# Optimization experiments

Measured on AMD Instinct MI355X. Metric: run time of the kernel, lower is better.

Reference implementation:

```python
import jax, jax.numpy as jnp
import numpy as np
import math

ANCHORS = np.array([[12., 16.], [19., 36.], [40., 28.]], dtype=np.float32)
NUM_CLASSES = 80
IMG_DIM = 608.0
NUM_ANCHORS = 3


def setup_inputs() -> dict:
    key = jax.random.key(0)
    ks = jax.random.split(key, 9)
    B, A, G, NC = 16, NUM_ANCHORS, 76, NUM_CLASSES
    x = jax.random.normal(ks[0], (B, A * (NC + 5), G, G), jnp.float32)
    iou = jax.random.uniform(ks[1], (B, A, G, G), jnp.float32, 0.0, 0.95)
    obj_mask = jax.random.bernoulli(ks[2], 0.02, (B, A, G, G))
    noobj_mask = jnp.logical_and(~obj_mask, jax.random.bernoulli(ks[3], 0.95, (B, A, G, G)))
    tw = jax.random.uniform(ks[4], (B, A, G, G), jnp.float32, 0.1, 4.0)
    th = jax.random.uniform(ks[5], (B, A, G, G), jnp.float32, 0.1, 4.0)
    tcls = jax.random.uniform(ks[6], (B, A, G, G, NC), jnp.float32)
    tconf = jax.random.uniform(ks[7], (B, A, G, G), jnp.float32)
    tb = jax.random.uniform(ks[8], (B, A, G, G, 4), jnp.float32)
    # target boxes in grid units: centers in [0,G), sizes in (0.5, 8.5)
    target_boxes = jnp.concatenate([tb[..., :2] * G, tb[..., 2:] * 8.0 + 0.5], -1)
    return {"x": x, "iou": iou, "obj_mask": obj_mask, "noobj_mask": noobj_mask,
            "tw": tw, "th": th, "tcls": tcls, "tconf": tconf, "target_boxes": target_boxes}


def _clog(p):
    # torch F.binary_cross_entropy clamps log to -100
    return jnp.maximum(jnp.log(p), -100.0)


def _bce(p, t):
    return -(t * _clog(p) + (1.0 - t) * _clog(1.0 - p))


def yolo_forward(x, iou, obj_mask, noobj_mask, tw, th, tcls, tconf, target_boxes):
    B = x.shape[0]
    G = x.shape[2]
    A, NC = NUM_ANCHORS, NUM_CLASSES
    stride = IMG_DIM / G
    # [B, A, G, G, 5+NC]
    pred = x.reshape(B, A, NC + 5, G, G).transpose(0, 1, 3, 4, 2)
    px = jax.nn.sigmoid(pred[..., 0])
    py = jax.nn.sigmoid(pred[..., 1])
    pw = pred[..., 2]
    ph = pred[..., 3]
    pconf = jax.nn.sigmoid(pred[..., 4])
    pcls = jax.nn.sigmoid(pred[..., 5:])

    scaled = jnp.asarray(ANCHORS) / stride
    gx = jnp.arange(G, dtype=x.dtype)[None, None, None, :]
    gy = jnp.arange(G, dtype=x.dtype)[None, None, :, None]
    aw = scaled[:, 0][None, :, None, None]
    ah = scaled[:, 1][None, :, None, None]

    bx = px + gx
    by = py + gy
    bw = jnp.exp(pw) * aw
    bh = jnp.exp(ph) * ah
    pred_boxes = jnp.stack([bx, by, bw, bh], -1)

    output = jnp.concatenate([
        pred_boxes.reshape(B, -1, 4) * stride,
        pconf.reshape(B, -1, 1),
        pcls.reshape(B, -1, NC)], -1)

    # ---- loss (masked CIoU + BCE), computed dense then mask-reduced ----
    m = obj_mask.astype(x.dtype)
    nm = noobj_mask.astype(x.dtype)
    txc, tyc, twd, tht = (target_boxes[..., i] for i in range(4))

    tx1, ty1 = txc - twd / 2, tyc - tht / 2
    tx2, ty2 = txc + twd / 2, tyc + tht / 2
    px1, py1 = bx - bw / 2, by - bh / 2
    px2, py2 = bx + bw / 2, by + bh / 2

    xc1 = jnp.minimum(px1, tx1)
    yc1 = jnp.minimum(py1, ty1)
    xc2 = jnp.maximum(px2, tx2)
    yc2 = jnp.maximum(py2, ty2)

    c = (xc2 - xc1) ** 2 + (yc2 - yc1) ** 2 + 1e-07
    d = (txc - bx) ** 2 + (tyc - by) ** 2
    rDIoU = d / c
    v = (4.0 / math.pi ** 2) * (jnp.arctan(tw / th) - jnp.arctan(pw / ph)) ** 2
    S = 1.0 - iou
    alpha = jax.lax.stop_gradient(v / (S + v))  # torch.no_grad() block
    ciou_term = 1.0 - iou + rDIoU + alpha * v
    CIoUloss = jnp.sum(m * ciou_term) / B

    cnt_obj = jnp.maximum(jnp.sum(m), 1.0)
    cnt_noobj = jnp.maximum(jnp.sum(nm), 1.0)
    bce_conf = _bce(pconf, tconf)
    loss_conf = 1.0 * jnp.sum(m * bce_conf) / cnt_obj + 100.0 * jnp.sum(nm * bce_conf) / cnt_noobj
    loss_cls = jnp.sum(m[..., None] * _bce(pcls, tcls)) / (cnt_obj * NUM_CLASSES)

    total_loss = CIoUloss + loss_conf + loss_cls
    return output, total_loss


def reference(x, iou, obj_mask, noobj_mask, tw, th, tcls, tconf, target_boxes):
    return yolo_forward(x, iou, obj_mask, noobj_mask, tw, th, tcls, tconf, target_boxes)
```

## Files before the change

kernel.cpp:

```cpp
#include <hip/hip_runtime.h>

#define B_ 16
#define A_ 3
#define G_ 76
#define GG_ (G_*G_)
#define NC_ 80
#define C_ 85
#define NCELL (B_*A_*GG_)
#define OUTN ((size_t)NCELL*C_)
#define NBLKM (NCELL/64)

typedef float f4 __attribute__((ext_vector_type(4)));

__device__ __forceinline__ float sigf(float v){ return 1.0f/(1.0f + __expf(-v)); }
__device__ __forceinline__ float clog_(float p){ return fmaxf(__logf(p), -100.0f); }
__device__ __forceinline__ float bcef(float p, float t){ return -(t*clog_(p) + (1.0f-t)*clog_(1.0f-p)); }

__global__ __launch_bounds__(256, 7) void mega_kernel(
        const float* __restrict__ x, const float* __restrict__ iou,
        const unsigned int* __restrict__ om, const unsigned int* __restrict__ nm,
        const float* __restrict__ tw, const float* __restrict__ th,
        const float* __restrict__ tcls, const float* __restrict__ tconf,
        const float* __restrict__ tbox,
        float* __restrict__ out, float* __restrict__ partials){
    __shared__ __align__(16) float lds[4][16*C_];
    __shared__ float sred[4][6];

    const int tid  = (int)threadIdx.x;
    const int w    = tid >> 6;
    const int lane = tid & 63;
    const int kg   = lane >> 4;
    const int ci   = lane & 15;

    unsigned qq = NBLKM >> 3, rr = NBLKM & 7u;
    unsigned xcd = blockIdx.x & 7u, seq = blockIdx.x >> 3;
    int blk = (int)((xcd < rr ? xcd*(qq+1u) : rr*(qq+1u) + (xcd-rr)*qq) + seq);

    int n0 = blk*64 + w*16;
    int n  = n0 + ci;
    int ba = n / GG_;
    int ij = n - ba*GG_;
    int a  = ba % A_;
    int in_ = ij / G_;
    int jn  = ij - in_*G_;
    const float* xb = x + (size_t)ba*C_*GG_ + (size_t)ij;
    float* ldsw = lds[w];

    bool obj   = om[n] != 0u;
    bool noobj = nm[n] != 0u;

    const float* tcl = tcls + (size_t)n*NC_;
    float aw8 = (a==0)?12.0f:((a==1)?19.0f:40.0f);
    float ah8 = (a==0)?16.0f:((a==1)?36.0f:28.0f);

    float clsacc = 0.f;
    float pb0=0.f, pb1=0.f, pb2=0.f, pb3=0.f, rwv=0.f, rhv=0.f, pcf=0.f;

    const float* p = xb + (size_t)(4*kg)*GG_;
    #pragma unroll
    for (int it=0; it<5; ++it){
        float e0 = p[0];
        float e1 = p[(size_t)GG_];
        float e2 = p[(size_t)2*GG_];
        float e3 = p[(size_t)3*GG_];
        int kb = 16*it + 4*kg;
        float r0,r1,r2,r3;
        if (it==0 && kg==0){
            float s0 = sigf(e0), s1 = sigf(e1);
            r0 = (s0 + (float)jn)*8.0f;
            r1 = (s1 + (float)in_)*8.0f;
            r2 = __expf(e2)*aw8;
            r3 = __expf(e3)*ah8;
            pb0=r0; pb1=r1; pb2=r2; pb3=r3; rwv=e2; rhv=e3;
        } else {
            r0 = sigf(e0); r1 = sigf(e1); r2 = sigf(e2); r3 = sigf(e3);
            if (it==0 && kg==1) pcf = r0;
            if (obj){
                if (kb+0 >= 5) clsacc += bcef(r0, tcl[kb-5]);
                if (kb+1 >= 5) clsacc += bcef(r1, tcl[kb-4]);
                if (kb+2 >= 5) clsacc += bcef(r2, tcl[kb-3]);
                if (kb+3 >= 5) clsacc += bcef(r3, tcl[kb-2]);
            }
        }
        int bix = ci*C_ + kb;
        ldsw[bix+0] = r0;
        ldsw[bix+1] = r1;
        ldsw[bix+2] = r2;
        ldsw[bix+3] = r3;
        p += (size_t)16*GG_;
    }
    if (kg == 0){
        float e0=p[0], e1=p[(size_t)GG_], e2=p[(size_t)2*GG_], e3=p[(size_t)3*GG_];
        float q0=sigf(e0), q1=sigf(e1), q2=sigf(e2), q3=sigf(e3);
        int bix = ci*C_ + 80;
        ldsw[bix+0]=q0; ldsw[bix+1]=q1; ldsw[bix+2]=q2; ldsw[bix+3]=q3;
        if (obj) clsacc += bcef(q0,tcl[75]) + bcef(q1,tcl[76]) + bcef(q2,tcl[77]) + bcef(q3,tcl[78]);
    } else if (kg == 1){
        float e4 = p[0];
        float q4 = sigf(e4);
        ldsw[ci*C_ + 84] = q4;
        if (obj) clsacc += bcef(q4, tcl[79]);
    }

    {
        float* outw = out + (size_t)n0*C_;
        const f4* src4 = (const f4*)ldsw;
        f4* dst4 = (f4*)outw;
        #pragma unroll
        for (int itb=0; itb<6; ++itb){
            int f = lane + itb*64;
            if (f < 340) dst4[f] = src4[f];
        }
    }

    float ciou=0.f, co=0.f, cn=0.f;
    if (kg==0 && obj){
        float iouv = iou[n], twv = tw[n], thv = th[n];
        f4 tb = *(const f4*)(tbox + (size_t)n*4);
        float bx = pb0*0.125f, by = pb1*0.125f, bw = pb2*0.125f, bh = pb3*0.125f;
        float txc=tb[0], tyc=tb[1], twd=tb[2], tht=tb[3];
        float tx1 = txc - twd*0.5f, ty1 = tyc - tht*0.5f;
        float tx2 = txc + twd*0.5f, ty2 = tyc + tht*0.5f;
        float px1 = bx - bw*0.5f,  py1 = by - bh*0.5f;
        float px2 = bx + bw*0.5f,  py2 = by + bh*0.5f;
        float xc1 = fminf(px1, tx1), yc1 = fminf(py1, ty1);
        float xc2 = fmaxf(px2, tx2), yc2 = fmaxf(py2, ty2);
        float cc = (xc2-xc1)*(xc2-xc1) + (yc2-yc1)*(yc2-yc1) + 1e-7f;
        float dd = (txc-bx)*(txc-bx) + (tyc-by)*(tyc-by);
        float rdiou = dd/cc;
        float dat = atanf(twv/thv) - atanf(rwv/rhv);
        float vv = 0.40528473456935108577f * dat*dat;
        float Si = 1.0f - iouv;
        float alpha = vv/(Si+vv);
        ciou = 1.0f - iouv + rdiou + alpha*vv;
    }
    if (kg==1 && (obj || noobj)){
        float bc = bcef(pcf, tconf[n]);
        co = obj ? bc : 0.f;
        cn = noobj ? bc : 0.f;
    }
    unsigned long long bo  = __ballot(obj)   & 0x00000000FFFF0000ULL;
    unsigned long long bn2 = __ballot(noobj) & 0x00000000FFFF0000ULL;

    float vals[4] = {ciou, co, cn, clsacc};
    #pragma unroll
    for (int q2=0; q2<4; ++q2){
        float v = vals[q2];
        #pragma unroll
        for (int o=32; o>0; o>>=1) v += __shfl_xor(v, o, 64);
        vals[q2] = v;
    }
    if (lane == 0){
        sred[w][0]=vals[0]; sred[w][1]=vals[1]; sred[w][2]=vals[2]; sred[w][3]=vals[3];
        sred[w][4]=(float)__popcll(bo); sred[w][5]=(float)__popcll(bn2);
    }
    __syncthreads();
    if (tid < 6)
        partials[(size_t)tid*NBLKM + blk] = sred[0][tid]+sred[1][tid]+sred[2][tid]+sred[3][tid];
}

__global__ __launch_bounds__(256) void final_kernel(const float* __restrict__ partials,
                                                    float* __restrict__ out_loss){
    double acc[6] = {0,0,0,0,0,0};
    for (int idx = (int)threadIdx.x; idx < NBLKM; idx += 256){
        #pragma unroll
        for (int q=0;q<6;q++) acc[q] += (double)partials[(size_t)q*NBLKM + idx];
    }
    #pragma unroll
    for (int q=0;q<6;q++){
        double v = acc[q];
        #pragma unroll
        for (int o=32;o>0;o>>=1) v += __shfl_xor(v, o, 64);
        acc[q] = v;
    }
    __shared__ double smd[6][4];
    int lane = (int)threadIdx.x & 63, wid = (int)threadIdx.x >> 6;
    if (lane == 0){
        #pragma unroll
        for (int q=0;q<6;q++) smd[q][wid] = acc[q];
    }
    __syncthreads();
    if (threadIdx.x == 0){
        double s[6];
        #pragma unroll
        for (int q=0;q<6;q++) s[q] = smd[q][0]+smd[q][1]+smd[q][2]+smd[q][3];
        double cnt_o = fmax(s[4], 1.0);
        double cnt_n = fmax(s[5], 1.0);
        double total = s[0]/(double)B_
                     + s[1]/cnt_o
                     + 100.0*s[2]/cnt_n
                     + s[3]/(cnt_o*(double)NC_);
        *out_loss = (float)total;
    }
}

extern "C" void kernel_launch(void* const* d_in, const int* in_sizes, int n_in,
                              void* d_out, int out_size, void* d_ws, size_t ws_size,
                              hipStream_t stream){
    const float* x     = (const float*)d_in[0];
    const float* iou   = (const float*)d_in[1];
    const unsigned int* om = (const unsigned int*)d_in[2];
    const unsigned int* nm = (const unsigned int*)d_in[3];
    const float* tw    = (const float*)d_in[4];
    const float* th    = (const float*)d_in[5];
    const float* tcls  = (const float*)d_in[6];
    const float* tconf = (const float*)d_in[7];
    const float* tbox  = (const float*)d_in[8];
    float* out = (float*)d_out;

    float* partials = (float*)d_ws;

    mega_kernel<<<NBLKM, 256, 0, stream>>>(x, iou, om, nm, tw, th, tcls, tconf, tbox,
                                           out, partials);
    final_kernel<<<1, 256, 0, stream>>>(partials, out + OUTN);
}
```

Measured before the change: 48.92 us.

## Vectorize channel loads with float4 and decouple loss computation via block-wide LDS

Each thread now loads float4 vectors of four adjacent cells per channel instead of scalar loads, so the whole block stages 64 cells times 85 channels in one shared buffer before a block-wide barrier. The loss pass is reorganized so four threads per cell split the 80-class BCE and reduce with shuffles, reading the activated values back from LDS. Raw w/h logits are kept in a small side array for the CIoU term. This trades per-wavefront independence for a __syncthreads and a larger LDS footprint, and the occupancy hint drops from 7 to 6.

```diff
diff --git a/kernel.cpp b/kernel.cpp
--- a/kernel.cpp
+++ b/kernel.cpp
@@ -9,6 +9,7 @@
 #define NCELL (B_*A_*GG_)
 #define OUTN ((size_t)NCELL*C_)
 #define NBLKM (NCELL/64)
+#define NSLOT (C_*16)
 
 typedef float f4 __attribute__((ext_vector_type(4)));
 
@@ -16,108 +17,119 @@
 __device__ __forceinline__ float clog_(float p){ return fmaxf(__logf(p), -100.0f); }
 __device__ __forceinline__ float bcef(float p, float t){ return -(t*clog_(p) + (1.0f-t)*clog_(1.0f-p)); }
 
-__global__ __launch_bounds__(256, 7) void mega_kernel(
+__global__ __launch_bounds__(256, 6) void mega_kernel(
         const float* __restrict__ x, const float* __restrict__ iou,
         const unsigned int* __restrict__ om, const unsigned int* __restrict__ nm,
         const float* __restrict__ tw, const float* __restrict__ th,
         const float* __restrict__ tcls, const float* __restrict__ tconf,
         const float* __restrict__ tbox,
         float* __restrict__ out, float* __restrict__ partials){
-    __shared__ __align__(16) float lds[4][16*C_];
+    __shared__ __align__(16) float lds[64*C_];
+    __shared__ float praw[64][2];
     __shared__ float sred[4][6];
 
     const int tid  = (int)threadIdx.x;
     const int w    = tid >> 6;
     const int lane = tid & 63;
-    const int kg   = lane >> 4;
-    const int ci   = lane & 15;
-
-    unsigned qq = NBLKM >> 3, rr = NBLKM & 7u;
+
+    unsigned qd8 = NBLKM >> 3, rr = NBLKM & 7u;
     unsigned xcd = blockIdx.x & 7u, seq = blockIdx.x >> 3;
-    int blk = (int)((xcd < rr ? xcd*(qq+1u) : rr*(qq+1u) + (xcd-rr)*qq) + seq);
-
-    int n0 = blk*64 + w*16;
-    int n  = n0 + ci;
-    int ba = n / GG_;
-    int ij = n - ba*GG_;
-    int a  = ba % A_;
-    int in_ = ij / G_;
-    int jn  = ij - in_*G_;
-    const float* xb = x + (size_t)ba*C_*GG_ + (size_t)ij;
-    float* ldsw = lds[w];
-
+    int blk = (int)((xcd < rr ? xcd*(qd8+1u) : rr*(qd8+1u) + (xcd-rr)*qd8) + seq);
+    int n0 = blk*64;
+
+    f4 rv[6];
+    #pragma unroll
+    for (int it=0; it<6; ++it){
+        int idx = tid + it*256;
+        if (idx < NSLOT){
+            int k = idx >> 4, q = idx & 15;
+            int cell0 = n0 + 4*q;
+            int ba = cell0 / GG_;
+            int ij0 = cell0 - ba*GG_;
+            rv[it] = *(const f4*)(x + ((size_t)ba*C_ + (size_t)k)*GG_ + ij0);
+        }
+    }
+
+    #pragma unroll
+    for (int it=0; it<6; ++it){
+        int idx = tid + it*256;
+        if (idx < NSLOT){
+            int k = idx >> 4, q = idx & 15;
+            int cell0 = n0 + 4*q;
+            int ba = cell0 / GG_;
+            int ij0 = cell0 - ba*GG_;
+            int in_ = ij0 / G_;
+            int jn0 = ij0 - in_*G_;
+            int a = ba % A_;
+            int lc0 = 4*q;
+            f4 v = rv[it];
+            f4 r;
+            if (k >= 4){
+                r[0]=sigf(v[0]); r[1]=sigf(v[1]); r[2]=sigf(v[2]); r[3]=sigf(v[3]);
+            } else if (k == 0){
+                float j0 = (float)jn0;
+                r[0]=(sigf(v[0])+j0)*8.0f;      r[1]=(sigf(v[1])+j0+1.0f)*8.0f;
+                r[2]=(sigf(v[2])+j0+2.0f)*8.0f; r[3]=(sigf(v[3])+j0+3.0f)*8.0f;
+            } else if (k == 1){
+                float fi = (float)in_;
+                r[0]=(sigf(v[0])+fi)*8.0f; r[1]=(sigf(v[1])+fi)*8.0f;
+                r[2]=(sigf(v[2])+fi)*8.0f; r[3]=(sigf(v[3])+fi)*8.0f;
+            } else if (k == 2){
+                float aw8 = (a==0)?12.0f:((a==1)?19.0f:40.0f);
+                r[0]=__expf(v[0])*aw8; r[1]=__expf(v[1])*aw8;
+                r[2]=__expf(v[2])*aw8; r[3]=__expf(v[3])*aw8;
+                praw[lc0+0][0]=v[0]; praw[lc0+1][0]=v[1];
+                praw[lc0+2][0]=v[2]; praw[lc0+3][0]=v[3];
+            } else {
+                float ah8 = (a==0)?16.0f:((a==1)?36.0f:28.0f);
+                r[0]=__expf(v[0])*ah8; r[1]=__expf(v[1])*ah8;
+                r[2]=__expf(v[2])*ah8; r[3]=__expf(v[3])*ah8;
+                praw[lc0+0][1]=v[0]; praw[lc0+1][1]=v[1];
+                praw[lc0+2][1]=v[2]; praw[lc0+3][1]=v[3];
+            }
+            int bix = lc0*C_ + k;
+            lds[bix]       = r[0];
+            lds[bix+C_]    = r[1];
+            lds[bix+2*C_]  = r[2];
+            lds[bix+3*C_]  = r[3];
+        }
+    }
+    __syncthreads();
+
+    {
+        const f4* src4 = (const f4*)lds;
+        f4* dst4 = (f4*)(out + (size_t)n0*C_);
+        #pragma unroll
+        for (int it=0; it<6; ++it){
+            int f = tid + it*256;
+            if (f < NSLOT) dst4[f] = src4[f];
+        }
+    }
+
+    int lc = tid >> 2, qd = tid & 3;
+    int n  = n0 + lc;
     bool obj   = om[n] != 0u;
     bool noobj = nm[n] != 0u;
-
-    const float* tcl = tcls + (size_t)n*NC_;
-    float aw8 = (a==0)?12.0f:((a==1)?19.0f:40.0f);
-    float ah8 = (a==0)?16.0f:((a==1)?36.0f:28.0f);
-
-    float clsacc = 0.f;
-    float pb0=0.f, pb1=0.f, pb2=0.f, pb3=0.f, rwv=0.f, rhv=0.f, pcf=0.f;
-
-    const float* p = xb + (size_t)(4*kg)*GG_;
-    #pragma unroll
-    for (int it=0; it<5; ++it){
-        float e0 = p[0];
-        float e1 = p[(size_t)GG_];
-        float e2 = p[(size_t)2*GG_];
-        float e3 = p[(size_t)3*GG_];
-        int kb = 16*it + 4*kg;
-        float r0,r1,r2,r3;
-        if (it==0 && kg==0){
-            float s0 = sigf(e0), s1 = sigf(e1);
-            r0 = (s0 + (float)jn)*8.0f;
-            r1 = (s1 + (float)in_)*8.0f;
-            r2 = __expf(e2)*aw8;
-            r3 = __expf(e3)*ah8;
-            pb0=r0; pb1=r1; pb2=r2; pb3=r3; rwv=e2; rhv=e3;
-        } else {
-            r0 = sigf(e0); r1 = sigf(e1); r2 = sigf(e2); r3 = sigf(e3);
-            if (it==0 && kg==1) pcf = r0;
-            if (obj){
-                if (kb+0 >= 5) clsacc += bcef(r0, tcl[kb-5]);
-                if (kb+1 >= 5) clsacc += bcef(r1, tcl[kb-4]);
-                if (kb+2 >= 5) clsacc += bcef(r2, tcl[kb-3]);
-                if (kb+3 >= 5) clsacc += bcef(r3, tcl[kb-2]);
-            }
-        }
-        int bix = ci*C_ + kb;
-        ldsw[bix+0] = r0;
-        ldsw[bix+1] = r1;
-        ldsw[bix+2] = r2;
-        ldsw[bix+3] = r3;
-        p += (size_t)16*GG_;
-    }
-    if (kg == 0){
-        float e0=p[0], e1=p[(size_t)GG_], e2=p[(size_t)2*GG_], e3=p[(size_t)3*GG_];
-        float q0=sigf(e0), q1=sigf(e1), q2=sigf(e2), q3=sigf(e3);
-        int bix = ci*C_ + 80;
-        ldsw[bix+0]=q0; ldsw[bix+1]=q1; ldsw[bix+2]=q2; ldsw[bix+3]=q3;
-        if (obj) clsacc += bcef(q0,tcl[75]) + bcef(q1,tcl[76]) + bcef(q2,tcl[77]) + bcef(q3,tcl[78]);
-    } else if (kg == 1){
-        float e4 = p[0];
-        float q4 = sigf(e4);
-        ldsw[ci*C_ + 84] = q4;
-        if (obj) clsacc += bcef(q4, tcl[79]);
-    }
-
-    {
-        float* outw = out + (size_t)n0*C_;
-        const f4* src4 = (const f4*)ldsw;
-        f4* dst4 = (f4*)outw;
-        #pragma unroll
-        for (int itb=0; itb<6; ++itb){
-            int f = lane + itb*64;
-            if (f < 340) dst4[f] = src4[f];
-        }
-    }
+    const float* lrow = lds + lc*C_;
+
+    float cls = 0.f;
+    if (obj){
+        const float* tcl = tcls + (size_t)n*NC_ + qd*20;
+        const float* lp  = lrow + 5 + qd*20;
+        #pragma unroll 4
+        for (int j=0; j<20; ++j) cls += bcef(lp[j], tcl[j]);
+    }
+    cls += __shfl_xor(cls, 1, 64);
+    cls += __shfl_xor(cls, 2, 64);
+    if (qd != 0) cls = 0.f;
 
     float ciou=0.f, co=0.f, cn=0.f;
-    if (kg==0 && obj){
+    if (qd == 0 && obj){
+        float bx = lrow[0]*0.125f, by = lrow[1]*0.125f;
+        float bw = lrow[2]*0.125f, bh = lrow[3]*0.125f;
+        float rwv = praw[lc][0], rhv = praw[lc][1];
         float iouv = iou[n], twv = tw[n], thv = th[n];
         f4 tb = *(const f4*)(tbox + (size_t)n*4);
-        float bx = pb0*0.125f, by = pb1*0.125f, bw = pb2*0.125f, bh = pb3*0.125f;
         float txc=tb[0], tyc=tb[1], twd=tb[2], tht=tb[3];
         float tx1 = txc - twd*0.5f, ty1 = tyc - tht*0.5f;
         float tx2 = txc + twd*0.5f, ty2 = tyc + tht*0.5f;
@@ -134,15 +146,15 @@
         float alpha = vv/(Si+vv);
         ciou = 1.0f - iouv + rdiou + alpha*vv;
     }
-    if (kg==1 && (obj || noobj)){
-        float bc = bcef(pcf, tconf[n]);
+    if (qd == 1 && (obj || noobj)){
+        float bc = bcef(lrow[4], tconf[n]);
         co = obj ? bc : 0.f;
         cn = noobj ? bc : 0.f;
     }
-    unsigned long long bo  = __ballot(obj)   & 0x00000000FFFF0000ULL;
-    unsigned long long bn2 = __ballot(noobj) & 0x00000000FFFF0000ULL;
-
-    float vals[4] = {ciou, co, cn, clsacc};
+    unsigned long long bo  = __ballot(obj   && qd == 0);
+    unsigned long long bn2 = __ballot(noobj && qd == 1);
+
+    float vals[4] = {ciou, co, cn, cls};
     #pragma unroll
     for (int q2=0; q2<4; ++q2){
         float v = vals[q2];
```

Measured after the change: 49.08 us. Within noise of the previous version (+0.3%).
